# Optimization experiments

Measured on AMD Instinct MI355X. Metric: run time of the kernel, lower is better.

The kernel has to match this reference:

```python
import jax, jax.numpy as jnp
import numpy as np

B, S, D, H, V, L, N, FF = 4, 2048, 768, 4, 32000, 2048, 3, 1024
DH = D // H  # 192; note original scales scores by 1/20, not 1/sqrt(192)


def layernorm(x, g, b):
    m = jnp.mean(x, axis=-1, keepdims=True)
    v = jnp.mean((x - m) ** 2, axis=-1, keepdims=True)
    return (x - m) / jnp.sqrt(v + 1e-5) * g + b


def attn_block(h, Wq, bq, Wk, bk, Wv, bv, g, b, mask):
    Bx, Sx, _ = h.shape
    q = (h @ Wq + bq).reshape(Bx, Sx, H, DH).transpose(0, 2, 1, 3)  # bhsd
    k = (h @ Wk + bk).reshape(Bx, Sx, H, DH).transpose(0, 2, 1, 3)
    v = (h @ Wv + bv).reshape(Bx, Sx, H, DH).transpose(0, 2, 1, 3)
    w = jnp.einsum('bhqd,bhkd->bhqk', q, k) / 20.0
    w = jnp.where(mask, -1e9, w)
    # original code uses Softmax(dim=2), i.e. over the QUERY axis — kept faithful
    a = jax.nn.softmax(w, axis=2)
    o = jnp.einsum('bhqk,bhkd->bhqd', a, v)
    o = o.transpose(0, 2, 1, 3).reshape(Bx, Sx, D)
    return layernorm(h + o, g, b)


def setup_inputs() -> dict:
    key = jax.random.key(0)
    ks = jax.random.split(key, 12)
    sc = 0.02
    n = lambda k, s: jax.random.normal(k, s, jnp.float32) * sc
    return {
        'x': jax.random.randint(ks[0], (B, S), 0, V),
        'label': jax.random.randint(ks[1], (B, S), 0, V),
        'tok_emb': n(ks[2], (V, D)),
        'pos_emb': n(ks[3], (L, D)),
        'Wq': n(ks[4], (N, 2, D, D)), 'bq': jnp.zeros((N, 2, D)),
        'Wk': n(ks[5], (N, 2, D, D)), 'bk': jnp.zeros((N, 2, D)),
        'Wv': n(ks[6], (N, 2, D, D)), 'bv': jnp.zeros((N, 2, D)),
        'ln_g': jnp.ones((N, 2, D)), 'ln_b': jnp.zeros((N, 2, D)),
        'W1': n(ks[7], (N, D, FF)), 'b1': jnp.zeros((N, FF)),
        'W2': n(ks[8], (N, FF, D)), 'b2': jnp.zeros((N, D)),
        'f_g': jnp.ones((N, D)), 'f_b': jnp.zeros((N, D)),
        'Wcls': n(ks[9], (D, V)), 'bcls': jnp.zeros((V,)),
    }


def reference(x, label, tok_emb, pos_emb, Wq, bq, Wk, bk, Wv, bv, ln_g, ln_b,
              W1, b1, W2, b2, f_g, f_b, Wcls, bcls):
    Bx, Sx = x.shape
    pad = (x == 0)[:, None, :, None]                       # [B,1,S,1] masks query rows
    look = jnp.triu(jnp.ones((Sx, Sx), bool), 1)[None, None]
    mask = look | pad                                      # [B,1,S,S] -> broadcast over H
    h = tok_emb[x] + pos_emb[jnp.arange(Sx)][None, :, :]
    for i in range(N):
        for j in range(2):
            h = attn_block(h, Wq[i, j], bq[i, j], Wk[i, j], bk[i, j],
                           Wv[i, j], bv[i, j], ln_g[i, j], ln_b[i, j], mask)
        h1 = jax.nn.relu(h @ W1[i] + b1[i]) @ W2[i] + b2[i]
        h = layernorm(h + h1, f_g[i], f_b[i])
    logits = h @ Wcls + bcls                               # [B,S,V]
    logp = jax.nn.log_softmax(logits, axis=-1)
    loss = -jnp.mean(jnp.take_along_axis(logp, label[..., None], axis=-1))
    return loss
```

## Files before the change

### kernel.cpp

```cpp
#include <hip/hip_runtime.h>
#include <hip/hip_bf16.h>

using u16 = unsigned short;
using u32 = unsigned int;
using u8  = unsigned char;
using u64 = unsigned long long;
using bf16x8 = __attribute__((ext_vector_type(8))) short;
using f32x4  = __attribute__((ext_vector_type(4))) float;
using l2v    = __attribute__((ext_vector_type(2))) long;

namespace {
constexpr int BB   = 4;
constexpr int SEQ  = 2048;
constexpr int DIM  = 768;
constexpr int NH   = 4;
constexpr int DHD  = 192;
constexpr int VOC  = 32000;
constexpr int NLAY = 3;
constexpr int FFD  = 1024;
constexpr int ROWS = BB * SEQ;
constexpr int NT2  = VOC / 256;
constexpr int QKV = 3 * DIM;
constexpr int BH  = BB * NH;
}

__device__ __forceinline__ float b2f(u16 u) { return __uint_as_float(((u32)u) << 16); }
__device__ __forceinline__ u16 f2b(float f) {
    u32 x = __float_as_uint(f);
    return (u16)((x + 0x7fffu + ((x >> 16) & 1u)) >> 16);
}

__device__ __forceinline__ u32 f2e4m3(float f) {
    float af = fabsf(f);
    u32 sgn = (__float_as_uint(f) >> 24) & 0x80u;
    if (!(af < 448.f)) return sgn | 0x7Eu;
    int e = (int)((__float_as_uint(af) >> 23) & 0xff) - 127;
    if (e < -6) e = -6;
    float sc = __uint_as_float((u32)(130 - e) << 23);
    int code = __float2int_rn(af * sc) + ((e + 6) << 3);
    return sgn | (u32)code;
}

__device__ __forceinline__ void gload16(const u16* g, u16* l) {
    __builtin_amdgcn_global_load_lds(
        (const __attribute__((address_space(1))) u32*)g,
        (__attribute__((address_space(3))) u32*)l, 16, 0, 0);
}
__device__ __forceinline__ void gload16b(const u8* g, u8* l) {
    __builtin_amdgcn_global_load_lds(
        (const __attribute__((address_space(1))) u32*)g,
        (__attribute__((address_space(3))) u32*)l, 16, 0, 0);
}

#define PHASE_END(N) do {                                        \
    __builtin_amdgcn_sched_barrier(0);                           \
    asm volatile("s_waitcnt vmcnt(" #N ")" ::: "memory");        \
    __builtin_amdgcn_s_barrier();                                \
    asm volatile("" ::: "memory");                               \
    __builtin_amdgcn_sched_barrier(0);                           \
} while (0)

__device__ __forceinline__ float block_sum256(float v, float* sb) {
    #pragma unroll
    for (int off = 32; off > 0; off >>= 1) v += __shfl_down(v, off, 64);
    int lane = threadIdx.x & 63, w = threadIdx.x >> 6;
    if (lane == 0) sb[w] = v;
    __syncthreads();
    float r = sb[0] + sb[1] + sb[2] + sb[3];
    __syncthreads();
    return r;
}

template<int MODE>
__global__ __launch_bounds__(512, 2)
void gemm256(const u16* __restrict__ A, long lda,
             const u16* __restrict__ Bt, long ldb,
             int M, int N, int K,
             u16* __restrict__ Cb, long ldc,
             int HH, long sAb, long sAh, long sBb, long sBh, long sCb, long sCh,
             const int* __restrict__ xtok, float* __restrict__ cpart)
{
    __shared__ __align__(16) u16 sA[2][256 * 64];
    __shared__ __align__(16) u16 sB[2][256 * 64];

    int t = threadIdx.x, w = t >> 6, lane = t & 63;
    int wr = w >> 2, wcn = w & 3;
    int lr = lane & 15, lg = lane >> 4, rsw = lr & 7;

    int z = blockIdx.z;
    int bz = z / HH, hz = z % HH;
    const u16* Ab = A + (size_t)bz * sAb + (size_t)hz * sAh;
    const u16* Bb = Bt + (size_t)bz * sBb + (size_t)hz * sBh;
    size_t Coff = (size_t)bz * sCb + (size_t)hz * sCh;

    int bx = blockIdx.x, by = blockIdx.y;
    {
        int tix = blockIdx.x;
        by = 7;
        while (by * (by + 1) / 2 > tix) by--;
        bx = tix - by * (by + 1) / 2;
    }
    int m0 = by * 256, n0 = bx * 256;

    int srow = lane >> 3;
    int scol = ((lane & 7) ^ srow) * 8;

    f32x4 acc[8][4];
    #pragma unroll
    for (int i = 0; i < 8; i++)
        #pragma unroll
        for (int j = 0; j < 4; j++) acc[i][j] = (f32x4){0.f, 0.f, 0.f, 0.f};

    auto stageA = [&](int buf, int k0) {
        #pragma unroll
        for (int r = 0; r < 4; r++) {
            int rb = r * 64 + w * 8;
            gload16(Ab + (size_t)(m0 + rb + srow) * lda + k0 + scol,
                    &sA[buf][rb * 64]);
        }
    };
    auto stageB = [&](int buf, int k0, int h) {
        #pragma unroll
        for (int j = 0; j < 2; j++) {
            int rb = (j * 2 + (w >> 2)) * 64 + h * 32 + (w & 3) * 8;
            gload16(Bb + (size_t)(n0 + rb + srow) * ldb + k0 + scol,
                    &sB[buf][rb * 64]);
        }
    };

    {
        int nt = K >> 6;
        stageA(0, 0); stageB(0, 0, 0); stageB(0, 0, 1);
        PHASE_END(0);

        for (int kt = 0; kt < nt; ++kt) {
            int cur = kt & 1;
            int kn = (kt + 1) << 6;
            bool st = (kt + 1 < nt);
            bf16x8 aa[2][8], bb[2][2];
            #pragma unroll
            for (int kx = 0; kx < 2; kx++) {
                int jsw = ((kx * 4 + lg) ^ rsw) * 8;
                #pragma unroll
                for (int mi = 0; mi < 8; mi++)
                    aa[kx][mi] = *(const bf16x8*)&sA[cur][(wr * 128 + mi * 16 + lr) * 64 + jsw];
                #pragma unroll
                for (int ni = 0; ni < 2; ni++)
                    bb[kx][ni] = *(const bf16x8*)&sB[cur][(wcn * 64 + ni * 16 + lr) * 64 + jsw];
            }
            if (st) { stageA(cur ^ 1, kn); stageB(cur ^ 1, kn, 0); }
            __builtin_amdgcn_s_setprio(1);
            #pragma unroll
            for (int kx = 0; kx < 2; kx++)
                #pragma unroll
                for (int mi = 0; mi < 8; mi++)
                    #pragma unroll
                    for (int ni = 0; ni < 2; ni++)
                        acc[mi][ni] = __builtin_amdgcn_mfma_f32_16x16x32_bf16(
                            aa[kx][mi], bb[kx][ni], acc[mi][ni], 0, 0, 0);
            __builtin_amdgcn_s_setprio(0);
            if (st) PHASE_END(6); else PHASE_END(0);

            bf16x8 bc[2][2];
            #pragma unroll
            for (int kx = 0; kx < 2; kx++) {
                int jsw = ((kx * 4 + lg) ^ rsw) * 8;
                #pragma unroll
                for (int ni = 0; ni < 2; ni++)
                    bc[kx][ni] = *(const bf16x8*)&sB[cur][(wcn * 64 + (ni + 2) * 16 + lr) * 64 + jsw];
            }
            if (st) stageB(cur ^ 1, kn, 1);
            __builtin_amdgcn_s_setprio(1);
            #pragma unroll
            for (int kx = 0; kx < 2; kx++)
                #pragma unroll
                for (int mi = 0; mi < 8; mi++)
                    #pragma unroll
                    for (int ni = 0; ni < 2; ni++)
                        acc[mi][ni + 2] = __builtin_amdgcn_mfma_f32_16x16x32_bf16(
                            aa[kx][mi], bc[kx][ni], acc[mi][ni + 2], 0, 0, 0);
            __builtin_amdgcn_s_setprio(0);
            if (st) PHASE_END(2); else PHASE_END(0);
        }
    }

    {
        const int* xb = xtok + (size_t)bz * SEQ;
        float cs[2][4] = {{0.f,0.f,0.f,0.f},{0.f,0.f,0.f,0.f}};
        #pragma unroll
        for (int mi = 0; mi < 8; mi++)
            #pragma unroll
            for (int j = 0; j < 4; j++) {
                int grow = m0 + wr * 128 + mi * 16 + lg * 4 + j;
                int xz = xb[grow];
                #pragma unroll
                for (int ni = 0; ni < 4; ni++) {
                    int gcol = n0 + wcn * 64 + ni * 16 + lr;
                    float v = acc[mi][ni][j] * 0.05f;
                    if (gcol > grow || xz == 0) v = -30.f;
                    float e = __expf(v);
                    Cb[Coff + (size_t)grow * ldc + gcol] = f2b(e);
                    cs[mi >> 2][ni] += e;
                }
            }
        #pragma unroll
        for (int h = 0; h < 2; h++)
            #pragma unroll
            for (int ni = 0; ni < 4; ni++) {
                float c = cs[h][ni];
                c += __shfl_xor(c, 16, 64);
                c += __shfl_xor(c, 32, 64);
                if (lg == 0) {
                    int p = (m0 >> 6) + wr * 2 + h;
                    cpart[((size_t)p * BH + z) * SEQ + n0 + wcn * 64 + ni * 16 + lr] = c;
                }
            }
    }
}

__global__ __launch_bounds__(512, 2)
void gemm256_f8(const u8* __restrict__ Aq, const u8* __restrict__ Bq, int K,
                const float* __restrict__ bias,
                const int* __restrict__ label,
                float* __restrict__ partials, float* __restrict__ picked)
{
    __shared__ __align__(16) u8 sA8[2][256 * 128];
    __shared__ __align__(16) u8 sB8[2][2][128 * 128];

    int t = threadIdx.x, w = t >> 6, lane = t & 63;
    int wr = w >> 2, wcn = w & 3;
    int lr = lane & 15, lg = lane >> 4;
    int rx = lr & 7;

    int bx = blockIdx.x, by = blockIdx.y;
    {
        int pid = by * gridDim.x + bx;
        int xcd = pid & 7, s = pid >> 3;
        bx = s >> 2;
        by = xcd * 4 + (s & 3);
    }
    int m0 = by * 256, n0 = bx * 256;

    int srow8 = lane >> 3;
    int scol8 = ((lane & 7) ^ srow8) * 16;

    f32x4 acc[8][4];
    #pragma unroll
    for (int i = 0; i < 8; i++)
        #pragma unroll
        for (int j = 0; j < 4; j++) acc[i][j] = (f32x4){0.f, 0.f, 0.f, 0.f};

    auto stageA = [&](int buf, int k0) {
        #pragma unroll
        for (int i = 0; i < 4; i++) {
            int rb = i * 64 + w * 8;
            gload16b(Aq + (size_t)(m0 + rb + srow8) * DIM + k0 + scol8,
                     &sA8[buf][rb * 128]);
        }
    };
    auto stageB = [&](int buf, int k0, int h) {
        #pragma unroll
        for (int j = 0; j < 2; j++) {
            int rh = j * 64 + w * 8;
            int rbase = (rh >> 5) * 64 + h * 32 + (rh & 31);
            gload16b(Bq + (size_t)(n0 + rbase + srow8) * DIM + k0 + scol8,
                     &sB8[buf][h][rh * 128]);
        }
    };

    int nt = K >> 7;
    stageA(0, 0); stageB(0, 0, 0); stageB(0, 0, 1);
    PHASE_END(0);

    for (int kt = 0; kt < nt; ++kt) {
        int cur = kt & 1;
        int kn = (kt + 1) << 7;
        bool st = (kt + 1 < nt);
        l2v aa[2][8], bb[2][2];
        #pragma unroll
        for (int h = 0; h < 2; h++) {
            int off = ((2 * lg + h) ^ rx) * 16;
            #pragma unroll
            for (int mi = 0; mi < 8; mi++)
                aa[h][mi] = *(const l2v*)&sA8[cur][(wr * 128 + mi * 16 + lr) * 128 + off];
            #pragma unroll
            for (int ni = 0; ni < 2; ni++)
                bb[h][ni] = *(const l2v*)&sB8[cur][0][(wcn * 32 + ni * 16 + lr) * 128 + off];
        }
        if (st) { stageA(cur ^ 1, kn); stageB(cur ^ 1, kn, 0); }
        __builtin_amdgcn_s_setprio(1);
        #pragma unroll
        for (int h = 0; h < 2; h++)
            #pragma unroll
            for (int e = 0; e < 2; e++)
                #pragma unroll
                for (int mi = 0; mi < 8; mi++)
                    #pragma unroll
                    for (int ni = 0; ni < 2; ni++)
                        acc[mi][ni] = __builtin_amdgcn_mfma_f32_16x16x32_fp8_fp8(
                            aa[h][mi][e], bb[h][ni][e], acc[mi][ni], 0, 0, 0);
        __builtin_amdgcn_s_setprio(0);
        if (st) PHASE_END(6); else PHASE_END(0);
        l2v bc[2][2];
        #pragma unroll
        for (int h = 0; h < 2; h++) {
            int off = ((2 * lg + h) ^ rx) * 16;
            #pragma unroll
            for (int ni = 0; ni < 2; ni++)
                bc[h][ni] = *(const l2v*)&sB8[cur][1][(wcn * 32 + ni * 16 + lr) * 128 + off];
        }
        if (st) stageB(cur ^ 1, kn, 1);
        __builtin_amdgcn_s_setprio(1);
        #pragma unroll
        for (int h = 0; h < 2; h++)
            #pragma unroll
            for (int e = 0; e < 2; e++)
                #pragma unroll
                for (int mi = 0; mi < 8; mi++)
                    #pragma unroll
                    for (int ni = 0; ni < 2; ni++)
                        acc[mi][ni + 2] = __builtin_amdgcn_mfma_f32_16x16x32_fp8_fp8(
                            aa[h][mi][e], bc[h][ni][e], acc[mi][ni + 2], 0, 0, 0);
        __builtin_amdgcn_s_setprio(0);
        if (st) PHASE_END(2); else PHASE_END(0);
    }

    #pragma unroll
    for (int mi = 0; mi < 8; mi++)
        #pragma unroll
        for (int ni = 0; ni < 4; ni++) {
            int gcol = n0 + wcn * 64 + ni * 16 + lr;
            float bcol = bias[gcol];
            #pragma unroll
            for (int j = 0; j < 4; j++)
                acc[mi][ni][j] = acc[mi][ni][j] * (1.f / 64.f) + bcol;
        }
    #pragma unroll
    for (int mi = 0; mi < 8; mi++)
        #pragma unroll
        for (int j = 0; j < 4; j++) {
            int grow = m0 + wr * 128 + mi * 16 + lg * 4 + j;
            int lab = label[grow];
            #pragma unroll
            for (int ni = 0; ni < 4; ni++) {
                int gcol = n0 + wcn * 64 + ni * 16 + lr;
                if (lab == gcol) picked[grow] = acc[mi][ni][j];
            }
        }
    float* red = (float*)sA8;
    #pragma unroll
    for (int mi = 0; mi < 8; mi++)
        #pragma unroll
        for (int j = 0; j < 4; j++) {
            float mx = -1e30f;
            #pragma unroll
            for (int ni = 0; ni < 4; ni++) mx = fmaxf(mx, acc[mi][ni][j]);
            #pragma unroll
            for (int off = 1; off < 16; off <<= 1)
                mx = fmaxf(mx, __shfl_xor(mx, off, 64));
            float ss = 0.f;
            #pragma unroll
            for (int ni = 0; ni < 4; ni++) ss += __expf(acc[mi][ni][j] - mx);
            #pragma unroll
            for (int off = 1; off < 16; off <<= 1) ss += __shfl_xor(ss, off, 64);
            if (lr == 0) {
                int rloc = wr * 128 + mi * 16 + lg * 4 + j;
                red[rloc * 8 + wcn * 2 + 0] = mx;
                red[rloc * 8 + wcn * 2 + 1] = ss;
            }
        }
    __syncthreads();
    if (t < 256) {
        float Mv = -1e30f;
        #pragma unroll
        for (int q = 0; q < 4; q++) Mv = fmaxf(Mv, red[t * 8 + q * 2]);
        float Sv = 0.f;
        #pragma unroll
        for (int q = 0; q < 4; q++)
            Sv += red[t * 8 + q * 2 + 1] * __expf(red[t * 8 + q * 2] - Mv);
        size_t row = (size_t)(m0 + t);
        partials[(row * NT2 + bx) * 2 + 0] = Mv;
        partials[(row * NT2 + bx) * 2 + 1] = Sv;
    }
}

__global__ __launch_bounds__(256)
void gemm128_f8(const u8* __restrict__ Aq, const u8* __restrict__ Bq,
                int K,
                const float* __restrict__ bias,
                u16* __restrict__ Cb, u8* __restrict__ Cq, long ldc, int relu)
{
    __shared__ __align__(16) u8 sA8[2][128 * 128];
    __shared__ __align__(16) u8 sB8[2][2][64 * 128];

    int t = threadIdx.x, w = t >> 6, lane = t & 63;
    int wr = w >> 1, wc = w & 1;
    int lr = lane & 15, lg = lane >> 4;
    int rx = lr & 7;

    int bx = blockIdx.x, by = blockIdx.y;
    {
        int pid = by * gridDim.x + bx;
        int xcd = pid & 7, s = pid >> 3;
        bx = s >> 3;
        by = xcd * 8 + (s & 7);
    }
    int m0 = by * 128, n0 = bx * 128;

    int srow8 = lane >> 3;
    int scol8 = ((lane & 7) ^ srow8) * 16;

    f32x4 acc[4][4];
    #pragma unroll
    for (int i = 0; i < 4; i++)
        #pragma unroll
        for (int j = 0; j < 4; j++) acc[i][j] = (f32x4){0.f, 0.f, 0.f, 0.f};

    auto stageA = [&](int buf, int k0) {
        #pragma unroll
        for (int i = 0; i < 4; i++) {
            int rb = i * 32 + w * 8;
            gload16b(Aq + (size_t)(m0 + rb + srow8) * K + k0 + scol8,
                     &sA8[buf][rb * 128]);
        }
    };
    auto stageB = [&](int buf, int k0, int h) {
        #pragma unroll
        for (int j = 0; j < 2; j++) {
            int rh = j * 32 + w * 8;
            int rbase = j * 64 + h * 32 + w * 8;
            gload16b(Bq + (size_t)(n0 + rbase + srow8) * K + k0 + scol8,
                     &sB8[buf][h][rh * 128]);
        }
    };

    int nt = K >> 7;
    stageA(0, 0); stageB(0, 0, 0); stageB(0, 0, 1);
    PHASE_END(0);

    for (int kt = 0; kt < nt; ++kt) {
        int cur = kt & 1;
        int kn = (kt + 1) << 7;
        bool st = (kt + 1 < nt);
        l2v aa[2][4], bb[2][2];
        #pragma unroll
        for (int h = 0; h < 2; h++) {
            int off = ((2 * lg + h) ^ rx) * 16;
            #pragma unroll
            for (int mi = 0; mi < 4; mi++)
                aa[h][mi] = *(const l2v*)&sA8[cur][(wr * 64 + mi * 16 + lr) * 128 + off];
            #pragma unroll
            for (int ni = 0; ni < 2; ni++)
                bb[h][ni] = *(const l2v*)&sB8[cur][0][(wc * 32 + ni * 16 + lr) * 128 + off];
        }
        if (st) { stageA(cur ^ 1, kn); stageB(cur ^ 1, kn, 0); }
        __builtin_amdgcn_s_setprio(1);
        #pragma unroll
        for (int h = 0; h < 2; h++)
            #pragma unroll
            for (int e = 0; e < 2; e++)
                #pragma unroll
                for (int mi = 0; mi < 4; mi++)
                    #pragma unroll
                    for (int ni = 0; ni < 2; ni++)
                        acc[mi][ni] = __builtin_amdgcn_mfma_f32_16x16x32_fp8_fp8(
                            aa[h][mi][e], bb[h][ni][e], acc[mi][ni], 0, 0, 0);
        __builtin_amdgcn_s_setprio(0);
        if (st) PHASE_END(6); else PHASE_END(0);
        l2v bc[2][2];
        #pragma unroll
        for (int h = 0; h < 2; h++) {
            int off = ((2 * lg + h) ^ rx) * 16;
            #pragma unroll
            for (int ni = 0; ni < 2; ni++)
                bc[h][ni] = *(const l2v*)&sB8[cur][1][(wc * 32 + ni * 16 + lr) * 128 + off];
        }
        if (st) stageB(cur ^ 1, kn, 1);
        __builtin_amdgcn_s_setprio(1);
        #pragma unroll
        for (int h = 0; h < 2; h++)
            #pragma unroll
            for (int e = 0; e < 2; e++)
                #pragma unroll
                for (int mi = 0; mi < 4; mi++)
                    #pragma unroll
                    for (int ni = 0; ni < 2; ni++)
                        acc[mi][ni + 2] = __builtin_amdgcn_mfma_f32_16x16x32_fp8_fp8(
                            aa[h][mi][e], bc[h][ni][e], acc[mi][ni + 2], 0, 0, 0);
        __builtin_amdgcn_s_setprio(0);
        if (st) PHASE_END(2); else PHASE_END(0);
    }

    #pragma unroll
    for (int mi = 0; mi < 4; mi++)
        #pragma unroll
        for (int ni = 0; ni < 4; ni++)
            #pragma unroll
            for (int j = 0; j < 4; j++) {
                int grow = m0 + wr * 64 + mi * 16 + lg * 4 + j;
                int gcol = n0 + wc * 64 + ni * 16 + lr;
                float v = acc[mi][ni][j] * (1.f / 64.f) + bias[gcol];
                if (relu) v = fmaxf(v, 0.f);
                size_t ci = (size_t)grow * ldc + gcol;
                if (Cb) Cb[ci] = f2b(v);
                if (Cq) Cq[ci] = (u8)f2e4m3(v * 4.f);
            }
}

template<int MODE>
__global__ __launch_bounds__(256)
void gemm128(const u16* __restrict__ A, long lda,
             const u16* __restrict__ Bt, long ldb,
             int N, int K,
             const float* __restrict__ bias,
             u16* __restrict__ Cb, long ldc, int relu,
             int HH, long sAb, long sAh, long sBb, long sBh, long sCb, long sCh)
{
    __shared__ __align__(16) u16 sA[2][128 * 64];
    __shared__ __align__(16) u16 sB[2][128 * 64];

    int z = blockIdx.z, bz = z / HH, hz = z % HH;
    const u16* Ab = A + (size_t)bz * sAb + (size_t)hz * sAh;
    const u16* Bb = Bt + (size_t)bz * sBb + (size_t)hz * sBh;
    size_t Coff = (size_t)bz * sCb + (size_t)hz * sCh;

    int bx = blockIdx.x, by = blockIdx.y;
    if (MODE == 3) {
        by = (by & 1) ? (15 - (by >> 1)) : (by >> 1);
    }
    int m0 = by * 128, n0 = bx * 128;

    int t = threadIdx.x, w = t >> 6, lane = t & 63;
    int wr = w >> 1, wc = w & 1, lr = lane & 15, lg = lane >> 4, rsw = lr & 7;
    int srow = lane >> 3, scol = ((lane & 7) ^ srow) * 8;

    f32x4 acc[4][4];
    #pragma unroll
    for (int i = 0; i < 4; i++)
        #pragma unroll
        for (int j = 0; j < 4; j++) acc[i][j] = (f32x4){0.f, 0.f, 0.f, 0.f};

    auto stageA = [&](int buf, int k0) {
        #pragma unroll
        for (int i = 0; i < 4; i++) {
            int rb = (w * 4 + i) * 8;
            gload16(Ab + (size_t)(m0 + rb + srow) * lda + k0 + scol,
                    &sA[buf][rb * 64]);
        }
    };
    auto stageB = [&](int buf, int k0, int h) {
        #pragma unroll
        for (int j = 0; j < 2; j++) {
            int rb = j * 64 + h * 32 + w * 8;
            int row = n0 + rb + srow;
            if (MODE == 3) { if (row > N - 1) row = N - 1; }
            gload16(Bb + (size_t)row * ldb + k0 + scol, &sB[buf][rb * 64]);
        }
    };

    int nt = K >> 6;
    if (MODE == 3) {
        int ntE = (by + 1) * 2;
        if (ntE < nt) nt = ntE;
    }

    stageA(0, 0); stageB(0, 0, 0); stageB(0, 0, 1);
    PHASE_END(0);

    for (int kt = 0; kt < nt; ++kt) {
        int cur = kt & 1;
        int kn = (kt + 1) << 6;
        bool st = (kt + 1 < nt);
        bf16x8 aa[2][4], bb[2][2];
        #pragma unroll
        for (int kx = 0; kx < 2; kx++) {
            int jsw = ((kx * 4 + lg) ^ rsw) * 8;
            #pragma unroll
            for (int mi = 0; mi < 4; mi++)
                aa[kx][mi] = *(const bf16x8*)&sA[cur][(wr * 64 + mi * 16 + lr) * 64 + jsw];
            #pragma unroll
            for (int ni = 0; ni < 2; ni++)
                bb[kx][ni] = *(const bf16x8*)&sB[cur][(wc * 64 + ni * 16 + lr) * 64 + jsw];
        }
        if (st) { stageA(cur ^ 1, kn); stageB(cur ^ 1, kn, 0); }
        __builtin_amdgcn_s_setprio(1);
        #pragma unroll
        for (int kx = 0; kx < 2; kx++)
            #pragma unroll
            for (int mi = 0; mi < 4; mi++)
                #pragma unroll
                for (int ni = 0; ni < 2; ni++)
                    acc[mi][ni] = __builtin_amdgcn_mfma_f32_16x16x32_bf16(
                        aa[kx][mi], bb[kx][ni], acc[mi][ni], 0, 0, 0);
        __builtin_amdgcn_s_setprio(0);
        if (st) PHASE_END(6); else PHASE_END(0);

        bf16x8 bc[2][2];
        #pragma unroll
        for (int kx = 0; kx < 2; kx++) {
            int jsw = ((kx * 4 + lg) ^ rsw) * 8;
            #pragma unroll
            for (int ni = 0; ni < 2; ni++)
                bc[kx][ni] = *(const bf16x8*)&sB[cur][(wc * 64 + (ni + 2) * 16 + lr) * 64 + jsw];
        }
        if (st) stageB(cur ^ 1, kn, 1);
        __builtin_amdgcn_s_setprio(1);
        #pragma unroll
        for (int kx = 0; kx < 2; kx++)
            #pragma unroll
            for (int mi = 0; mi < 4; mi++)
                #pragma unroll
                for (int ni = 0; ni < 2; ni++)
                    acc[mi][ni + 2] = __builtin_amdgcn_mfma_f32_16x16x32_bf16(
                        aa[kx][mi], bc[kx][ni], acc[mi][ni + 2], 0, 0, 0);
        __builtin_amdgcn_s_setprio(0);
        if (st) PHASE_END(2); else PHASE_END(0);
    }

    #pragma unroll
    for (int mi = 0; mi < 4; mi++)
        #pragma unroll
        for (int ni = 0; ni < 4; ni++)
            #pragma unroll
            for (int j = 0; j < 4; j++) {
                int grow = m0 + wr * 64 + mi * 16 + lg * 4 + j;
                int gcol = n0 + wc * 64 + ni * 16 + lr;
                if (gcol < N)
                    Cb[Coff + (size_t)grow * ldc + gcol] = f2b(acc[mi][ni][j]);
            }
}

__global__ __launch_bounds__(256)
void embed_k(const int* __restrict__ x, const float* __restrict__ tok,
             const float* __restrict__ pos, u16* __restrict__ hb, u8* __restrict__ hq)
{
    int row = blockIdx.x, t = threadIdx.x;
    int token = x[row];
    int s = row & (SEQ - 1);
    size_t base = (size_t)row * DIM;
    #pragma unroll
    for (int e = 0; e < 3; e++) {
        int d = t + e * 256;
        float v = tok[(size_t)token * DIM + d] + pos[(size_t)s * DIM + d];
        hb[base + d] = f2b(v);
        hq[base + d] = (u8)f2e4m3(v * 4.f);
    }
}

__global__ __launch_bounds__(256)
void resid_ln(const u16* __restrict__ res, const u16* __restrict__ add,
              const float* __restrict__ g, const float* __restrict__ b,
              u16* __restrict__ out, u8* __restrict__ outq)
{
    __shared__ float sb[4];
    int row = blockIdx.x, t = threadIdx.x;
    size_t base = (size_t)row * DIM;
    float x0 = 0.f, x1 = 0.f, x2 = 0.f, x3 = 0.f;
    if (t < 192) {
        ushort4 r4 = *(const ushort4*)&res[base + t * 4];
        ushort4 a4 = *(const ushort4*)&add[base + t * 4];
        x0 = b2f(r4.x) + b2f(a4.x);
        x1 = b2f(r4.y) + b2f(a4.y);
        x2 = b2f(r4.z) + b2f(a4.z);
        x3 = b2f(r4.w) + b2f(a4.w);
    }
    float mean = block_sum256(x0 + x1 + x2 + x3, sb) * (1.f / DIM);
    float d0 = x0 - mean, d1 = x1 - mean, d2 = x2 - mean, d3 = x3 - mean;
    float var = block_sum256(t < 192 ? d0*d0 + d1*d1 + d2*d2 + d3*d3 : 0.f, sb) * (1.f / DIM);
    float rs = rsqrtf(var + 1e-5f);
    if (t < 192) {
        float4 gv = *(const float4*)&g[t * 4];
        float4 bv = *(const float4*)&b[t * 4];
        float y0 = d0 * rs * gv.x + bv.x, y1 = d1 * rs * gv.y + bv.y;
        float y2 = d2 * rs * gv.z + bv.z, y3 = d3 * rs * gv.w + bv.w;
        ushort4 ob = {f2b(y0), f2b(y1), f2b(y2), f2b(y3)};
        *(ushort4*)&out[base + t * 4] = ob;
        uchar4 oq = {(u8)f2e4m3(y0 * 4.f), (u8)f2e4m3(y1 * 4.f),
                     (u8)f2e4m3(y2 * 4.f), (u8)f2e4m3(y3 * 4.f)};
        *(uchar4*)&outq[base + t * 4] = oq;
    }
}

__global__ void v_transpose(const u16* __restrict__ v, long ldv,
                            const float* __restrict__ cpart, u16* __restrict__ vT)
{
    __shared__ u16 tile[32][33];
    int z = blockIdx.z;
    int b = z >> 2, h = z & 3;
    int s0 = blockIdx.x * 32, d0 = blockIdx.y * 32;
    int tx = threadIdx.x, ty = threadIdx.y;
    #pragma unroll
    for (int i = 0; i < 4; i++)
        tile[ty + i * 8][tx] = v[((size_t)b * SEQ + s0 + ty + i * 8) * ldv + h * DHD + d0 + tx];
    int scol = s0 + tx;
    int pmin = (scol >> 8) * 4;
    float sv = 0.f;
    for (int p = pmin; p < 32; p++) sv += cpart[((size_t)p * BH + z) * SEQ + scol];
    float inv = 1.f / sv;
    __syncthreads();
    #pragma unroll
    for (int i = 0; i < 4; i++)
        vT[((size_t)z * DHD + d0 + ty + i * 8) * SEQ + scol] =
            f2b(b2f(tile[tx][ty + i * 8]) * inv);
}

__global__ void wt_cvt8_z(const float* __restrict__ src0, long sSrc,
                          u8* __restrict__ dst0, long sDst, int K, int N)
{
    __shared__ float tile[32][33];
    const float* src = src0 + (size_t)blockIdx.z * sSrc;
    u8* dst = dst0 + (size_t)blockIdx.z * sDst;
    int n0 = blockIdx.x * 32, k0 = blockIdx.y * 32;
    int tx = threadIdx.x, ty = threadIdx.y;
    #pragma unroll
    for (int i = 0; i < 4; i++)
        tile[ty + i * 8][tx] = src[(size_t)(k0 + ty + i * 8) * N + n0 + tx];
    __syncthreads();
    #pragma unroll
    for (int i = 0; i < 4; i++)
        dst[(size_t)(n0 + ty + i * 8) * K + k0 + tx] =
            (u8)f2e4m3(tile[tx][ty + i * 8] * 16.f);
}

__global__ __launch_bounds__(256)
void bias_cat(const float* __restrict__ bq, const float* __restrict__ bk,
              const float* __restrict__ bv, float* __restrict__ dst)
{
    int ij = blockIdx.x, t = threadIdx.x;
    #pragma unroll
    for (int e = 0; e < 3; e++) {
        int d = t + e * 256;
        dst[(size_t)ij * QKV + d]            = bq[(size_t)ij * DIM + d];
        dst[(size_t)ij * QKV + DIM + d]      = bk[(size_t)ij * DIM + d];
        dst[(size_t)ij * QKV + 2 * DIM + d]  = bv[(size_t)ij * DIM + d];
    }
}

__global__ __launch_bounds__(256)
void lse_merge(const float* __restrict__ partials, float* __restrict__ lse)
{
    __shared__ float sm[4], ssum[4];
    int row = blockIdx.x, t = threadIdx.x;
    float m = -1e30f, s = 0.f;
    if (t < NT2) {
        const float* p = partials + ((size_t)row * NT2 + t) * 2;
        m = p[0]; s = p[1];
    }
    #pragma unroll
    for (int off = 1; off < 64; off <<= 1) {
        float om = __shfl_xor(m, off, 64), os = __shfl_xor(s, off, 64);
        float M = fmaxf(m, om);
        s = s * __expf(m - M) + os * __expf(om - M);
        m = M;
    }
    int lane = t & 63, w = t >> 6;
    if (lane == 0) { sm[w] = m; ssum[w] = s; }
    __syncthreads();
    if (t == 0) {
        float M = fmaxf(fmaxf(sm[0], sm[1]), fmaxf(sm[2], sm[3]));
        float S = ssum[0] * __expf(sm[0] - M) + ssum[1] * __expf(sm[1] - M) +
                  ssum[2] * __expf(sm[2] - M) + ssum[3] * __expf(sm[3] - M);
        lse[row] = M + __logf(S);
    }
}

__global__ __launch_bounds__(256)
void loss_k(const float* __restrict__ lse, const float* __restrict__ picked,
            float* __restrict__ out)
{
    __shared__ float sb[4];
    int t = threadIdx.x;
    float a = 0.f;
    for (int r = t; r < ROWS; r += 256) a += lse[r] - picked[r];
    float tot = block_sum256(a, sb);
    if (t == 0) out[0] = tot / (float)ROWS;
}

extern "C" void kernel_launch(void* const* d_in, const int* in_sizes, int n_in,
                              void* d_out, int out_size, void* d_ws, size_t ws_size,
                              hipStream_t stream)
{
    (void)in_sizes; (void)n_in; (void)out_size; (void)ws_size;
    const int*   x     = (const int*)d_in[0];
    const int*   label = (const int*)d_in[1];
    const float* tok   = (const float*)d_in[2];
    const float* pos   = (const float*)d_in[3];
    const float* Wq    = (const float*)d_in[4];
    const float* bq    = (const float*)d_in[5];
    const float* Wk    = (const float*)d_in[6];
    const float* bk    = (const float*)d_in[7];
    const float* Wv    = (const float*)d_in[8];
    const float* bv    = (const float*)d_in[9];
    const float* ln_g  = (const float*)d_in[10];
    const float* ln_b  = (const float*)d_in[11];
    const float* W1    = (const float*)d_in[12];
    const float* b1    = (const float*)d_in[13];
    const float* W2    = (const float*)d_in[14];
    const float* b2    = (const float*)d_in[15];
    const float* f_g   = (const float*)d_in[16];
    const float* f_b   = (const float*)d_in[17];
    const float* Wcls  = (const float*)d_in[18];
    const float* bcls  = (const float*)d_in[19];

    char* p = (char*)d_ws;
    auto alloc = [&](size_t bytes) -> char* {
        char* r = p;
        p += (bytes + 255) & ~(size_t)255;
        return r;
    };
    u16* hb     = (u16*)alloc((size_t)ROWS * DIM * 2);
    u8*  hq     = (u8*)alloc((size_t)ROWS * DIM);
    u16* ob     = (u16*)alloc((size_t)ROWS * DIM * 2);
    u16* qkvb   = (u16*)alloc((size_t)ROWS * QKV * 2);
    u16* vTb    = (u16*)alloc((size_t)BH * DHD * SEQ * 2);
    u8*  ff1q   = (u8*)alloc((size_t)ROWS * FFD);
    u16* wbuf   = (u16*)alloc((size_t)BH * SEQ * SEQ * 2);
    u8*  WqkvT8 = (u8*)alloc((size_t)6 * QKV * DIM);
    u8*  W1T8   = (u8*)alloc((size_t)NLAY * DIM * FFD);
    u8*  W2T8   = (u8*)alloc((size_t)NLAY * FFD * DIM);
    u8*  WcT8   = (u8*)alloc((size_t)DIM * VOC);
    float* bqkv = (float*)alloc((size_t)6 * QKV * 4);
    float* cpart= (float*)alloc((size_t)32 * BH * SEQ * 4);
    float* partials = (float*)alloc((size_t)ROWS * NT2 * 2 * 4);
    float* picked   = (float*)alloc((size_t)ROWS * 4);
    float* lsev     = (float*)alloc((size_t)ROWS * 4);

    dim3 t32(32, 8, 1);
    wt_cvt8_z<<<dim3(DIM / 32, DIM / 32, 6), t32, 0, stream>>>(
        Wq, (long)DIM * DIM, WqkvT8, (long)QKV * DIM, DIM, DIM);
    wt_cvt8_z<<<dim3(DIM / 32, DIM / 32, 6), t32, 0, stream>>>(
        Wk, (long)DIM * DIM, WqkvT8 + (size_t)DIM * DIM, (long)QKV * DIM, DIM, DIM);
    wt_cvt8_z<<<dim3(DIM / 32, DIM / 32, 6), t32, 0, stream>>>(
        Wv, (long)DIM * DIM, WqkvT8 + (size_t)2 * DIM * DIM, (long)QKV * DIM, DIM, DIM);
    wt_cvt8_z<<<dim3(FFD / 32, DIM / 32, NLAY), t32, 0, stream>>>(
        W1, (long)DIM * FFD, W1T8, (long)DIM * FFD, DIM, FFD);
    wt_cvt8_z<<<dim3(DIM / 32, FFD / 32, NLAY), t32, 0, stream>>>(
        W2, (long)FFD * DIM, W2T8, (long)FFD * DIM, FFD, DIM);
    wt_cvt8_z<<<dim3(VOC / 32, DIM / 32, 1), t32, 0, stream>>>(
        Wcls, 0L, WcT8, 0L, DIM, VOC);
    bias_cat<<<6, 256, 0, stream>>>(bq, bk, bv, bqkv);

    embed_k<<<ROWS, 256, 0, stream>>>(x, tok, pos, hb, hq);

    for (int i = 0; i < NLAY; i++) {
        for (int j = 0; j < 2; j++) {
            int ij = i * 2 + j;
            gemm128_f8<<<dim3(QKV / 128, ROWS / 128, 1), 256, 0, stream>>>(
                hq, WqkvT8 + (size_t)ij * QKV * DIM, DIM,
                bqkv + (size_t)ij * QKV, qkvb, nullptr, QKV, 0);
            gemm256<1><<<dim3(36, 1, BH), 512, 0, stream>>>(
                qkvb, QKV, qkvb + DIM, QKV, SEQ, SEQ, DHD,
                wbuf, SEQ,
                NH, (long)SEQ * QKV, (long)DHD, (long)SEQ * QKV, (long)DHD,
                (long)NH * SEQ * SEQ, (long)SEQ * SEQ,
                x, cpart);
            v_transpose<<<dim3(SEQ / 32, DHD / 32, BH), t32, 0, stream>>>(
                qkvb + 2 * DIM, QKV, cpart, vTb);
            gemm128<3><<<dim3(2, SEQ / 128, BH), 256, 0, stream>>>(
                wbuf, SEQ, vTb, SEQ, DHD, SEQ,
                nullptr, ob, DIM, 0,
                NH, (long)NH * SEQ * SEQ, (long)SEQ * SEQ,
                (long)NH * DHD * SEQ, (long)DHD * SEQ,
                (long)SEQ * DIM, (long)DHD);
            resid_ln<<<ROWS, 256, 0, stream>>>(
                hb, ob, ln_g + (size_t)ij * DIM, ln_b + (size_t)ij * DIM, hb, hq);
        }
        gemm128_f8<<<dim3(FFD / 128, ROWS / 128, 1), 256, 0, stream>>>(
            hq, W1T8 + (size_t)i * DIM * FFD, DIM,
            b1 + (size_t)i * FFD, nullptr, ff1q, FFD, 1);
        gemm128_f8<<<dim3(DIM / 128, ROWS / 128, 1), 256, 0, stream>>>(
            ff1q, W2T8 + (size_t)i * FFD * DIM, FFD,
            b2 + (size_t)i * DIM, ob, nullptr, DIM, 0);
        resid_ln<<<ROWS, 256, 0, stream>>>(
            hb, ob, f_g + (size_t)i * DIM, f_b + (size_t)i * DIM, hb, hq);
    }

    gemm256_f8<<<dim3(NT2, ROWS / 256, 1), 512, 0, stream>>>(
        hq, WcT8, DIM, bcls, label, partials, picked);
    lse_merge<<<ROWS, 256, 0, stream>>>(partials, lsev);
    loss_k<<<1, 256, 0, stream>>>(lsev, picked, (float*)d_out);
}
```

Measured before the change: 1.727 ms.

## Run attention score and PV GEMMs in FP8 with quantized Q/K/V and probabilities

After: 1.764 ms. 2.1% more time.

```diff
diff --git a/kernel.cpp b/kernel.cpp
--- a/kernel.cpp
+++ b/kernel.cpp
@@ -40,12 +40,13 @@
     int code = __float2int_rn(af * sc) + ((e + 6) << 3);
     return sgn | (u32)code;
 }
-
-__device__ __forceinline__ void gload16(const u16* g, u16* l) {
-    __builtin_amdgcn_global_load_lds(
-        (const __attribute__((address_space(1))) u32*)g,
-        (__attribute__((address_space(3))) u32*)l, 16, 0, 0);
-}
+__device__ __forceinline__ float e4m3f(u8 v) {
+    int e = (v >> 3) & 15, m = v & 7;
+    float f = (e == 0) ? (float)m * 0.001953125f
+                       : __uint_as_float((u32)((e + 120) << 23) | ((u32)m << 20));
+    return (v & 0x80u) ? -f : f;
+}
+
 __device__ __forceinline__ void gload16b(const u8* g, u8* l) {
     __builtin_amdgcn_global_load_lds(
         (const __attribute__((address_space(1))) u32*)g,
@@ -71,39 +72,32 @@
     return r;
 }
 
-template<int MODE>
 __global__ __launch_bounds__(512, 2)
-void gemm256(const u16* __restrict__ A, long lda,
-             const u16* __restrict__ Bt, long ldb,
-             int M, int N, int K,
-             u16* __restrict__ Cb, long ldc,
-             int HH, long sAb, long sAh, long sBb, long sBh, long sCb, long sCh,
-             const int* __restrict__ xtok, float* __restrict__ cpart)
-{
-    __shared__ __align__(16) u16 sA[2][256 * 64];
-    __shared__ __align__(16) u16 sB[2][256 * 64];
+void gemm256s_f8(const u8* __restrict__ qkvq, const int* __restrict__ xtok,
+                 u8* __restrict__ Pq, float* __restrict__ cpart)
+{
+    __shared__ __align__(16) u8 sA8[2][256 * 64];
+    __shared__ __align__(16) u8 sB8[2][256 * 64];
 
     int t = threadIdx.x, w = t >> 6, lane = t & 63;
     int wr = w >> 2, wcn = w & 3;
-    int lr = lane & 15, lg = lane >> 4, rsw = lr & 7;
-
-    int z = blockIdx.z;
-    int bz = z / HH, hz = z % HH;
-    const u16* Ab = A + (size_t)bz * sAb + (size_t)hz * sAh;
-    const u16* Bb = Bt + (size_t)bz * sBb + (size_t)hz * sBh;
-    size_t Coff = (size_t)bz * sCb + (size_t)hz * sCh;
-
-    int bx = blockIdx.x, by = blockIdx.y;
+    int lr = lane & 15, lg = lane >> 4;
+
+    int z = blockIdx.z, bz = z >> 2, hz = z & 3;
+    const u8* Qb = qkvq + (size_t)bz * SEQ * QKV + hz * DHD;
+    const u8* Kb = Qb + DIM;
+    size_t Coff = (size_t)z * SEQ * SEQ;
+
+    int by = 7;
     {
         int tix = blockIdx.x;
-        by = 7;
         while (by * (by + 1) / 2 > tix) by--;
-        bx = tix - by * (by + 1) / 2;
-    }
+    }
+    int bx = blockIdx.x - by * (by + 1) / 2;
     int m0 = by * 256, n0 = bx * 256;
 
-    int srow = lane >> 3;
-    int scol = ((lane & 7) ^ srow) * 8;
+    int sr4 = lane >> 2;
+    int sc4 = ((lane & 3) ^ (sr4 & 3)) * 16;
 
     f32x4 acc[8][4];
     #pragma unroll
@@ -111,111 +105,81 @@
         #pragma unroll
         for (int j = 0; j < 4; j++) acc[i][j] = (f32x4){0.f, 0.f, 0.f, 0.f};
 
-    auto stageA = [&](int buf, int k0) {
-        #pragma unroll
-        for (int r = 0; r < 4; r++) {
-            int rb = r * 64 + w * 8;
-            gload16(Ab + (size_t)(m0 + rb + srow) * lda + k0 + scol,
-                    &sA[buf][rb * 64]);
+    auto stA = [&](int buf, int k0) {
+        #pragma unroll
+        for (int i = 0; i < 2; i++) {
+            int rb = i * 128 + w * 16;
+            gload16b(Qb + (size_t)(m0 + rb + sr4) * QKV + k0 + sc4,
+                     &sA8[buf][rb * 64]);
         }
     };
-    auto stageB = [&](int buf, int k0, int h) {
-        #pragma unroll
-        for (int j = 0; j < 2; j++) {
-            int rb = (j * 2 + (w >> 2)) * 64 + h * 32 + (w & 3) * 8;
-            gload16(Bb + (size_t)(n0 + rb + srow) * ldb + k0 + scol,
-                    &sB[buf][rb * 64]);
+    auto stB = [&](int buf, int k0) {
+        #pragma unroll
+        for (int i = 0; i < 2; i++) {
+            int rb = i * 128 + w * 16;
+            gload16b(Kb + (size_t)(n0 + rb + sr4) * QKV + k0 + sc4,
+                     &sB8[buf][rb * 64]);
         }
     };
 
-    {
-        int nt = K >> 6;
-        stageA(0, 0); stageB(0, 0, 0); stageB(0, 0, 1);
+    stA(0, 0); stB(0, 0);
+    PHASE_END(0);
+
+    #pragma unroll
+    for (int kt = 0; kt < 3; ++kt) {
+        int cur = kt & 1;
+        int off = (lg ^ (lr & 3)) * 16;
+        l2v a[8], b[4];
+        #pragma unroll
+        for (int mi = 0; mi < 8; mi++)
+            a[mi] = *(const l2v*)&sA8[cur][(wr * 128 + mi * 16 + lr) * 64 + off];
+        #pragma unroll
+        for (int ni = 0; ni < 4; ni++)
+            b[ni] = *(const l2v*)&sB8[cur][(wcn * 64 + ni * 16 + lr) * 64 + off];
+        if (kt < 2) { stA(cur ^ 1, (kt + 1) * 64); stB(cur ^ 1, (kt + 1) * 64); }
+        __builtin_amdgcn_s_setprio(1);
+        #pragma unroll
+        for (int e = 0; e < 2; e++)
+            #pragma unroll
+            for (int mi = 0; mi < 8; mi++)
+                #pragma unroll
+                for (int ni = 0; ni < 4; ni++)
+                    acc[mi][ni] = __builtin_amdgcn_mfma_f32_16x16x32_fp8_fp8(
+                        a[mi][e], b[ni][e], acc[mi][ni], 0, 0, 0);
+        __builtin_amdgcn_s_setprio(0);
         PHASE_END(0);
-
-        for (int kt = 0; kt < nt; ++kt) {
-            int cur = kt & 1;
-            int kn = (kt + 1) << 6;
-            bool st = (kt + 1 < nt);
-            bf16x8 aa[2][8], bb[2][2];
-            #pragma unroll
-            for (int kx = 0; kx < 2; kx++) {
-                int jsw = ((kx * 4 + lg) ^ rsw) * 8;
-                #pragma unroll
-                for (int mi = 0; mi < 8; mi++)
-                    aa[kx][mi] = *(const bf16x8*)&sA[cur][(wr * 128 + mi * 16 + lr) * 64 + jsw];
-                #pragma unroll
-                for (int ni = 0; ni < 2; ni++)
-                    bb[kx][ni] = *(const bf16x8*)&sB[cur][(wcn * 64 + ni * 16 + lr) * 64 + jsw];
+    }
+
+    const int* xb = xtok + (size_t)bz * SEQ;
+    float cs[2][4] = {{0.f,0.f,0.f,0.f},{0.f,0.f,0.f,0.f}};
+    #pragma unroll
+    for (int mi = 0; mi < 8; mi++)
+        #pragma unroll
+        for (int j = 0; j < 4; j++) {
+            int grow = m0 + wr * 128 + mi * 16 + lg * 4 + j;
+            int xz = xb[grow];
+            #pragma unroll
+            for (int ni = 0; ni < 4; ni++) {
+                int gcol = n0 + wcn * 64 + ni * 16 + lr;
+                float v = acc[mi][ni][j] * 0.003125f;
+                if (gcol > grow || xz == 0) v = -30.f;
+                float e = __expf(v);
+                Pq[Coff + (size_t)grow * SEQ + gcol] = (u8)f2e4m3(e * 16.f);
+                cs[mi >> 2][ni] += e;
             }
-            if (st) { stageA(cur ^ 1, kn); stageB(cur ^ 1, kn, 0); }
-            __builtin_amdgcn_s_setprio(1);
-            #pragma unroll
-            for (int kx = 0; kx < 2; kx++)
-                #pragma unroll
-                for (int mi = 0; mi < 8; mi++)
-                    #pragma unroll
-                    for (int ni = 0; ni < 2; ni++)
-                        acc[mi][ni] = __builtin_amdgcn_mfma_f32_16x16x32_bf16(
-                            aa[kx][mi], bb[kx][ni], acc[mi][ni], 0, 0, 0);
-            __builtin_amdgcn_s_setprio(0);
-            if (st) PHASE_END(6); else PHASE_END(0);
-
-            bf16x8 bc[2][2];
-            #pragma unroll
-            for (int kx = 0; kx < 2; kx++) {
-                int jsw = ((kx * 4 + lg) ^ rsw) * 8;
-                #pragma unroll
-                for (int ni = 0; ni < 2; ni++)
-                    bc[kx][ni] = *(const bf16x8*)&sB[cur][(wcn * 64 + (ni + 2) * 16 + lr) * 64 + jsw];
+        }
+    #pragma unroll
+    for (int h = 0; h < 2; h++)
+        #pragma unroll
+        for (int ni = 0; ni < 4; ni++) {
+            float c = cs[h][ni];
+            c += __shfl_xor(c, 16, 64);
+            c += __shfl_xor(c, 32, 64);
+            if (lg == 0) {
+                int p = (m0 >> 6) + wr * 2 + h;
+                cpart[((size_t)p * BH + z) * SEQ + n0 + wcn * 64 + ni * 16 + lr] = c;
             }
-            if (st) stageB(cur ^ 1, kn, 1);
-            __builtin_amdgcn_s_setprio(1);
-            #pragma unroll
-            for (int kx = 0; kx < 2; kx++)
-                #pragma unroll
-                for (int mi = 0; mi < 8; mi++)
-                    #pragma unroll
-                    for (int ni = 0; ni < 2; ni++)
-                        acc[mi][ni + 2] = __builtin_amdgcn_mfma_f32_16x16x32_bf16(
-                            aa[kx][mi], bc[kx][ni], acc[mi][ni + 2], 0, 0, 0);
-            __builtin_amdgcn_s_setprio(0);
-            if (st) PHASE_END(2); else PHASE_END(0);
-        }
-    }
-
-    {
-        const int* xb = xtok + (size_t)bz * SEQ;
-        float cs[2][4] = {{0.f,0.f,0.f,0.f},{0.f,0.f,0.f,0.f}};
-        #pragma unroll
-        for (int mi = 0; mi < 8; mi++)
-            #pragma unroll
-            for (int j = 0; j < 4; j++) {
-                int grow = m0 + wr * 128 + mi * 16 + lg * 4 + j;
-                int xz = xb[grow];
-                #pragma unroll
-                for (int ni = 0; ni < 4; ni++) {
-                    int gcol = n0 + wcn * 64 + ni * 16 + lr;
-                    float v = acc[mi][ni][j] * 0.05f;
-                    if (gcol > grow || xz == 0) v = -30.f;
-                    float e = __expf(v);
-                    Cb[Coff + (size_t)grow * ldc + gcol] = f2b(e);
-                    cs[mi >> 2][ni] += e;
-                }
-            }
-        #pragma unroll
-        for (int h = 0; h < 2; h++)
-            #pragma unroll
-            for (int ni = 0; ni < 4; ni++) {
-                float c = cs[h][ni];
-                c += __shfl_xor(c, 16, 64);
-                c += __shfl_xor(c, 32, 64);
-                if (lg == 0) {
-                    int p = (m0 >> 6) + wr * 2 + h;
-                    cpart[((size_t)p * BH + z) * SEQ + n0 + wcn * 64 + ni * 16 + lr] = c;
-                }
-            }
-    }
+        }
 }
 
 __global__ __launch_bounds__(512, 2)
@@ -467,6 +431,7 @@
                             aa[h][mi][e], bb[h][ni][e], acc[mi][ni], 0, 0, 0);
         __builtin_amdgcn_s_setprio(0);
         if (st) PHASE_END(6); else PHASE_END(0);
+
         l2v bc[2][2];
         #pragma unroll
         for (int h = 0; h < 2; h++) {
@@ -507,32 +472,29 @@
             }
 }
 
-template<int MODE>
 __global__ __launch_bounds__(256)
-void gemm128(const u16* __restrict__ A, long lda,
-             const u16* __restrict__ Bt, long ldb,
-             int N, int K,
-             const float* __restrict__ bias,
-             u16* __restrict__ Cb, long ldc, int relu,
-             int HH, long sAb, long sAh, long sBb, long sBh, long sCb, long sCh)
-{
-    __shared__ __align__(16) u16 sA[2][128 * 64];
-    __shared__ __align__(16) u16 sB[2][128 * 64];
-
-    int z = blockIdx.z, bz = z / HH, hz = z % HH;
-    const u16* Ab = A + (size_t)bz * sAb + (size_t)hz * sAh;
-    const u16* Bb = Bt + (size_t)bz * sBb + (size_t)hz * sBh;
-    size_t Coff = (size_t)bz * sCb + (size_t)hz * sCh;
+void gemm128pv_f8(const u8* __restrict__ Pq, const u8* __restrict__ vTq,
+                  u16* __restrict__ Cb)
+{
+    __shared__ __align__(16) u8 sA8[2][128 * 128];
+    __shared__ __align__(16) u8 sB8[2][2][64 * 128];
+
+    int t = threadIdx.x, w = t >> 6, lane = t & 63;
+    int wr = w >> 1, wc = w & 1;
+    int lr = lane & 15, lg = lane >> 4;
+    int rx = lr & 7;
+
+    int z = blockIdx.z, bz = z >> 2, hz = z & 3;
+    const u8* Ab = Pq + (size_t)z * SEQ * SEQ;
+    const u8* Bb = vTq + (size_t)z * DHD * SEQ;
+    size_t Coff = (size_t)bz * SEQ * DIM + (size_t)hz * DHD;
 
     int bx = blockIdx.x, by = blockIdx.y;
-    if (MODE == 3) {
-        by = (by & 1) ? (15 - (by >> 1)) : (by >> 1);
-    }
+    by = (by & 1) ? (15 - (by >> 1)) : (by >> 1);
     int m0 = by * 128, n0 = bx * 128;
 
-    int t = threadIdx.x, w = t >> 6, lane = t & 63;
-    int wr = w >> 1, wc = w & 1, lr = lane & 15, lg = lane >> 4, rsw = lr & 7;
-    int srow = lane >> 3, scol = ((lane & 7) ^ srow) * 8;
+    int srow8 = lane >> 3;
+    int scol8 = ((lane & 7) ^ srow8) * 16;
 
     f32x4 acc[4][4];
     #pragma unroll
@@ -543,76 +505,77 @@
     auto stageA = [&](int buf, int k0) {
         #pragma unroll
         for (int i = 0; i < 4; i++) {
-            int rb = (w * 4 + i) * 8;
-            gload16(Ab + (size_t)(m0 + rb + srow) * lda + k0 + scol,
-                    &sA[buf][rb * 64]);
+            int rb = i * 32 + w * 8;
+            gload16b(Ab + (size_t)(m0 + rb + srow8) * SEQ + k0 + scol8,
+                     &sA8[buf][rb * 128]);
         }
     };
     auto stageB = [&](int buf, int k0, int h) {
         #pragma unroll
         for (int j = 0; j < 2; j++) {
-            int rb = j * 64 + h * 32 + w * 8;
-            int row = n0 + rb + srow;
-            if (MODE == 3) { if (row > N - 1) row = N - 1; }
-            gload16(Bb + (size_t)row * ldb + k0 + scol, &sB[buf][rb * 64]);
+            int rh = j * 32 + w * 8;
+            int rbase = j * 64 + h * 32 + w * 8;
+            int row = n0 + rbase + srow8;
+            if (row > DHD - 1) row = DHD - 1;
+            gload16b(Bb + (size_t)row * SEQ + k0 + scol8,
+                     &sB8[buf][h][rh * 128]);
         }
     };
 
-    int nt = K >> 6;
-    if (MODE == 3) {
-        int ntE = (by + 1) * 2;
-        if (ntE < nt) nt = ntE;
-    }
-
+    int nt = by + 1;
     stageA(0, 0); stageB(0, 0, 0); stageB(0, 0, 1);
     PHASE_END(0);
 
     for (int kt = 0; kt < nt; ++kt) {
         int cur = kt & 1;
-        int kn = (kt + 1) << 6;
+        int kn = (kt + 1) << 7;
         bool st = (kt + 1 < nt);
-        bf16x8 aa[2][4], bb[2][2];
-        #pragma unroll
-        for (int kx = 0; kx < 2; kx++) {
-            int jsw = ((kx * 4 + lg) ^ rsw) * 8;
+        l2v aa[2][4], bb[2][2];
+        #pragma unroll
+        for (int h = 0; h < 2; h++) {
+            int off = ((2 * lg + h) ^ rx) * 16;
             #pragma unroll
             for (int mi = 0; mi < 4; mi++)
-                aa[kx][mi] = *(const bf16x8*)&sA[cur][(wr * 64 + mi * 16 + lr) * 64 + jsw];
+                aa[h][mi] = *(const l2v*)&sA8[cur][(wr * 64 + mi * 16 + lr) * 128 + off];
             #pragma unroll
             for (int ni = 0; ni < 2; ni++)
-                bb[kx][ni] = *(const bf16x8*)&sB[cur][(wc * 64 + ni * 16 + lr) * 64 + jsw];
+                bb[h][ni] = *(const l2v*)&sB8[cur][0][(wc * 32 + ni * 16 + lr) * 128 + off];
         }
         if (st) { stageA(cur ^ 1, kn); stageB(cur ^ 1, kn, 0); }
         __builtin_amdgcn_s_setprio(1);
         #pragma unroll
-        for (int kx = 0; kx < 2; kx++)
-            #pragma unroll
-            for (int mi = 0; mi < 4; mi++)
+        for (int h = 0; h < 2; h++)
+            #pragma unroll
+            for (int e = 0; e < 2; e++)
                 #pragma unroll
-                for (int ni = 0; ni < 2; ni++)
-                    acc[mi][ni] = __builtin_amdgcn_mfma_f32_16x16x32_bf16(
-                        aa[kx][mi], bb[kx][ni], acc[mi][ni], 0, 0, 0);
+                for (int mi = 0; mi < 4; mi++)
+                    #pragma unroll
+                    for (int ni = 0; ni < 2; ni++)
+                        acc[mi][ni] = __builtin_amdgcn_mfma_f32_16x16x32_fp8_fp8(
+                            aa[h][mi][e], bb[h][ni][e], acc[mi][ni], 0, 0, 0);
         __builtin_amdgcn_s_setprio(0);
         if (st) PHASE_END(6); else PHASE_END(0);
 
-        bf16x8 bc[2][2];
-        #pragma unroll
-        for (int kx = 0; kx < 2; kx++) {
-            int jsw = ((kx * 4 + lg) ^ rsw) * 8;
+        l2v bc[2][2];
+        #pragma unroll
+        for (int h = 0; h < 2; h++) {
+            int off = ((2 * lg + h) ^ rx) * 16;
             #pragma unroll
             for (int ni = 0; ni < 2; ni++)
-                bc[kx][ni] = *(const bf16x8*)&sB[cur][(wc * 64 + (ni + 2) * 16 + lr) * 64 + jsw];
+                bc[h][ni] = *(const l2v*)&sB8[cur][1][(wc * 32 + ni * 16 + lr) * 128 + off];
         }
         if (st) stageB(cur ^ 1, kn, 1);
         __builtin_amdgcn_s_setprio(1);
         #pragma unroll
-        for (int kx = 0; kx < 2; kx++)
-            #pragma unroll
-            for (int mi = 0; mi < 4; mi++)
+        for (int h = 0; h < 2; h++)
+            #pragma unroll
+            for (int e = 0; e < 2; e++)
                 #pragma unroll
-                for (int ni = 0; ni < 2; ni++)
-                    acc[mi][ni + 2] = __builtin_amdgcn_mfma_f32_16x16x32_bf16(
-                        aa[kx][mi], bc[kx][ni], acc[mi][ni + 2], 0, 0, 0);
+                for (int mi = 0; mi < 4; mi++)
+                    #pragma unroll
+                    for (int ni = 0; ni < 2; ni++)
+                        acc[mi][ni + 2] = __builtin_amdgcn_mfma_f32_16x16x32_fp8_fp8(
+                            aa[h][mi][e], bc[h][ni][e], acc[mi][ni + 2], 0, 0, 0);
         __builtin_amdgcn_s_setprio(0);
         if (st) PHASE_END(2); else PHASE_END(0);
     }
@@ -625,8 +588,9 @@
             for (int j = 0; j < 4; j++) {
                 int grow = m0 + wr * 64 + mi * 16 + lg * 4 + j;
                 int gcol = n0 + wc * 64 + ni * 16 + lr;
-                if (gcol < N)
-                    Cb[Coff + (size_t)grow * ldc + gcol] = f2b(acc[mi][ni][j]);
+                if (gcol < DHD)
+                    Cb[Coff + (size_t)grow * DIM + gcol] =
+                        f2b(acc[mi][ni][j] * (1.f / 256.f));
             }
 }
 
@@ -681,10 +645,10 @@
     }
 }
 
-__global__ void v_transpose(const u16* __restrict__ v, long ldv,
-                            const float* __restrict__ cpart, u16* __restrict__ vT)
-{
-    __shared__ u16 tile[32][33];
+__global__ void v_transpose(const u8* __restrict__ v, long ldv,
+                            const float* __restrict__ cpart, u8* __restrict__ vT)
+{
+    __shared__ u8 tile[32][33];
     int z = blockIdx.z;
     int b = z >> 2, h = z & 3;
     int s0 = blockIdx.x * 32, d0 = blockIdx.y * 32;
@@ -696,12 +660,12 @@
     int pmin = (scol >> 8) * 4;
     float sv = 0.f;
     for (int p = pmin; p < 32; p++) sv += cpart[((size_t)p * BH + z) * SEQ + scol];
-    float inv = 1.f / sv;
+    float sc = 4.f / sv;
     __syncthreads();
     #pragma unroll
     for (int i = 0; i < 4; i++)
         vT[((size_t)z * DHD + d0 + ty + i * 8) * SEQ + scol] =
-            f2b(b2f(tile[tx][ty + i * 8]) * inv);
+            (u8)f2e4m3(e4m3f(tile[tx][ty + i * 8]) * sc);
 }
 
 __global__ void wt_cvt8_z(const float* __restrict__ src0, long sSrc,
@@ -811,10 +775,10 @@
     u16* hb     = (u16*)alloc((size_t)ROWS * DIM * 2);
     u8*  hq     = (u8*)alloc((size_t)ROWS * DIM);
     u16* ob     = (u16*)alloc((size_t)ROWS * DIM * 2);
-    u16* qkvb   = (u16*)alloc((size_t)ROWS * QKV * 2);
-    u16* vTb    = (u16*)alloc((size_t)BH * DHD * SEQ * 2);
+    u8*  qkvq   = (u8*)alloc((size_t)ROWS * QKV);
+    u8*  vTq    = (u8*)alloc((size_t)BH * DHD * SEQ);
     u8*  ff1q   = (u8*)alloc((size_t)ROWS * FFD);
-    u16* wbuf   = (u16*)alloc((size_t)BH * SEQ * SEQ * 2);
+    u8*  wbufq  = (u8*)alloc((size_t)BH * SEQ * SEQ);
     u8*  WqkvT8 = (u8*)alloc((size_t)6 * QKV * DIM);
     u8*  W1T8   = (u8*)alloc((size_t)NLAY * DIM * FFD);
     u8*  W2T8   = (u8*)alloc((size_t)NLAY * FFD * DIM);
@@ -847,21 +811,13 @@
             int ij = i * 2 + j;
             gemm128_f8<<<dim3(QKV / 128, ROWS / 128, 1), 256, 0, stream>>>(
                 hq, WqkvT8 + (size_t)ij * QKV * DIM, DIM,
-                bqkv + (size_t)ij * QKV, qkvb, nullptr, QKV, 0);
-            gemm256<1><<<dim3(36, 1, BH), 512, 0, stream>>>(
-                qkvb, QKV, qkvb + DIM, QKV, SEQ, SEQ, DHD,
-                wbuf, SEQ,
-                NH, (long)SEQ * QKV, (long)DHD, (long)SEQ * QKV, (long)DHD,
-                (long)NH * SEQ * SEQ, (long)SEQ * SEQ,
-                x, cpart);
+                bqkv + (size_t)ij * QKV, nullptr, qkvq, QKV, 0);
+            gemm256s_f8<<<dim3(36, 1, BH), 512, 0, stream>>>(
+                qkvq, x, wbufq, cpart);
             v_transpose<<<dim3(SEQ / 32, DHD / 32, BH), t32, 0, stream>>>(
-                qkvb + 2 * DIM, QKV, cpart, vTb);
-            gemm128<3><<<dim3(2, SEQ / 128, BH), 256, 0, stream>>>(
-                wbuf, SEQ, vTb, SEQ, DHD, SEQ,
-                nullptr, ob, DIM, 0,
-                NH, (long)NH * SEQ * SEQ, (long)SEQ * SEQ,
-                (long)NH * DHD * SEQ, (long)DHD * SEQ,
-                (long)SEQ * DIM, (long)DHD);
+                qkvq + 2 * DIM, QKV, cpart, vTq);
+            gemm128pv_f8<<<dim3(2, SEQ / 128, BH), 256, 0, stream>>>(
+                wbufq, vTq, ob);
             resid_ln<<<ROWS, 256, 0, stream>>>(
                 hb, ob, ln_g + (size_t)ij * DIM, ln_b + (size_t)ij * DIM, hb, hq);
         }
```
